# Performance work log

Hardware: AMD Instinct MI355X
Metric: run time of the kernel (lower is better)

Reference implementation:

```python
import jax, jax.numpy as jnp
import numpy as np

K, D = 512, 256

def setup_inputs() -> dict:
    key = jax.random.key(0)
    k1, k2 = jax.random.split(key)
    z_e = jax.random.normal(k1, (64, D, 32, 32), dtype=jnp.float32)
    # matches nn.Embedding weight init uniform_(-1/K, 1/K)
    codebook = jax.random.uniform(k2, (K, D), dtype=jnp.float32, minval=-1.0 / K, maxval=1.0 / K)
    return {"z_e": z_e, "codebook": codebook}

def reference(z_e, codebook):
    N, Dd, H, W = z_e.shape
    # NCHW -> (N*H*W, D) tokens
    x = jnp.transpose(z_e, (0, 2, 3, 1)).reshape(-1, Dd)
    x_sq = jnp.sum(x * x, axis=1, keepdims=True)            # [T, 1]
    w_sq = jnp.sum(codebook * codebook, axis=1)             # [K]
    dists = x_sq - 2.0 * (x @ codebook.T) + w_sq[None, :]   # [T, K]
    q = jnp.argmin(dists, axis=1)                           # [T]
    z_q = codebook[q]                                       # [T, D] gather
    z_q = z_q.reshape(N, H, W, Dd).transpose(0, 3, 1, 2)    # back to NCHW
    q = q.reshape(N, H, W).astype(jnp.int64)
    return (q, z_q)
```

## Files before the change

kernel.cpp:

```cpp
#include <hip/hip_runtime.h>
#include <float.h>
#include <math.h>


#define KCODES 512
#define DDIM   256
#define HWSZ   1024
#define TTOK   65536
#define TPB    128
#define NBLK   (TTOK / TPB)
#define NCHUNK 16
#define MARGIN 3.0e-4f
#define KINIT  0x00800000u

#define HW_OFF 65536
#define BK_OFF 67584
#define LDS_SZ 68096
#define WLC_OFF 49152
#define WLT_OFF 49168
#define WLK_OFF 49680
#define ZQ_PITCH 528

typedef short bf16x8 __attribute__((ext_vector_type(8)));
typedef float f32x16 __attribute__((ext_vector_type(16)));
typedef float f32x4  __attribute__((ext_vector_type(4)));

__device__ inline unsigned short bf16rne(float x) {
    union { float f; unsigned u; } a; a.f = x;
    unsigned r = a.u + (0x7fffu + ((a.u >> 16) & 1u));
    return (unsigned short)(r >> 16);
}
__device__ inline float bf16tof(unsigned short h) {
    union { unsigned u; float f; } b; b.u = ((unsigned)h) << 16; return b.f;
}

__device__ inline unsigned enc_key(float f, int code) {
    unsigned s = __float_as_uint(f);
    unsigned u = (s & 0x80000000u) ? ~s : (s | 0x80000000u);
    return (u & 0xFFFFFE00u) | (unsigned)code;
}
__device__ inline float dec_key(unsigned k) {
    unsigned u = k & 0xFFFFFE00u;
    unsigned s = (u & 0x80000000u) ? (u & 0x7FFFFFFFu) : ~u;
    return __uint_as_float(s);
}

__device__ __forceinline__ void top4k(unsigned k, unsigned kb[4]) {
    #pragma unroll
    for (int l = 0; l < 4; ++l) {
        const unsigned mx = k > kb[l] ? k : kb[l];
        const unsigned mn = k > kb[l] ? kb[l] : k;
        kb[l] = mx; k = mn;
    }
}
__device__ __forceinline__ void top8k(unsigned k, unsigned kb[8]) {
    #pragma unroll
    for (int l = 0; l < 8; ++l) {
        const unsigned mx = k > kb[l] ? k : kb[l];
        const unsigned mn = k > kb[l] ? kb[l] : k;
        kb[l] = mx; k = mn;
    }
}

__global__ __launch_bounds__(256) void vq_prep(const float* __restrict__ cb,
                                               unsigned char* __restrict__ wsw,
                                               float* __restrict__ wsq) {
    const int tid = threadIdx.x;
    const int gid = blockIdx.x * 256 + tid;
    {
        const int k = gid >> 5, o = gid & 31;
        const int d0 = o * 8, c = o >> 1, half = o & 1;
        unsigned hi[4], lo[4];
        #pragma unroll
        for (int jj = 0; jj < 4; ++jj) {
            float v0 = cb[k * DDIM + d0 + 2 * jj];
            float v1 = cb[k * DDIM + d0 + 2 * jj + 1];
            unsigned short h0 = bf16rne(v0), h1 = bf16rne(v1);
            unsigned short l0 = bf16rne(v0 - bf16tof(h0));
            unsigned short l1 = bf16rne(v1 - bf16tof(h1));
            hi[jj] = (unsigned)h0 | ((unsigned)h1 << 16);
            lo[jj] = (unsigned)l0 | ((unsigned)l1 << 16);
        }
        const int tile = k >> 5, lane2 = (k & 31) + 32 * half;
        *(uint4*)(wsw + ((size_t)((c * 2 + 0) * 16 + tile) * 1024) + lane2 * 16) = make_uint4(hi[0], hi[1], hi[2], hi[3]);
        *(uint4*)(wsw + ((size_t)((c * 2 + 1) * 16 + tile) * 1024) + lane2 * 16) = make_uint4(lo[0], lo[1], lo[2], lo[3]);
    }
    if (blockIdx.x < 32) {
        const int k = blockIdx.x * 16 + (tid >> 4);
        const int s = tid & 15, h2 = s >> 3, j2 = s & 7;
        const float* p = cb + (size_t)k * DDIM + h2 * 128 + j2;
        float v[16];
        #pragma unroll
        for (int i = 0; i < 16; ++i) v[i] = p[i * 8];
        float rr;
        {
#pragma clang fp contract(off)
            rr = v[0] * v[0];
            #pragma unroll
            for (int i = 1; i < 16; ++i) { float sq = v[i] * v[i]; rr = rr + sq; }
        }
        float t = rr;
        t = t + __shfl_xor(t, 1);
        t = t + __shfl_xor(t, 2);
        t = t + __shfl_xor(t, 4);
        t = t + __shfl_xor(t, 8);
        if (s == 0) wsq[k] = t;
    }
}

__global__ __launch_bounds__(512, 4) void vq_main(const float* __restrict__ z_e,
                                                  const float* __restrict__ cb,
                                                  const float* __restrict__ wsq,
                                                  const unsigned char* __restrict__ wsw,
                                                  float* __restrict__ out) {
    __shared__ __align__(16) unsigned char lds[LDS_SZ];

    const int tid = threadIdx.x;
    const int wv = tid >> 6, lane = tid & 63;
    const int tbase = blockIdx.x * TPB;
    const int n = tbase >> 10, hw0 = tbase & (HWSZ - 1);
    const float* zb = z_e + (size_t)n * (DDIM * HWSZ) + hw0;

    {
        const int tok = tid & 127, g = tid >> 7;
        const int mtS = tok >> 5;
        const int lbase = (tok & 31) * 16;
        #pragma unroll
        for (int o = 0; o < 8; ++o) {
            const int d0 = g * 64 + o * 8;
            float v[8];
            #pragma unroll
            for (int j = 0; j < 8; ++j) v[j] = zb[(size_t)(d0 + j) * HWSZ + tok];
            unsigned hi[4];
            #pragma unroll
            for (int jj = 0; jj < 4; ++jj) {
                unsigned short h0 = bf16rne(v[2 * jj]), h1 = bf16rne(v[2 * jj + 1]);
                hi[jj] = (unsigned)h0 | ((unsigned)h1 << 16);
            }
            const int c = d0 >> 4;
            const int off2 = lbase + 512 * ((d0 >> 3) & 1);
            *(uint4*)(lds + (mtS * 16 + c) * 1024 + off2) = make_uint4(hi[0], hi[1], hi[2], hi[3]);
        }
    }
    ((float*)(lds + HW_OFF))[tid] = 0.5f * wsq[tid];

    __syncthreads();

    const int hh = lane >> 5;
    const int ct0 = wv * 2;
    const float* hwsqL = (const float*)(lds + HW_OFF);
    unsigned* candp = (unsigned*)lds;

    #define LDW(c, p, t)   (*(const bf16x8*)(wsw + ((size_t)(((c) * 2 + (p)) * 16 + (t)) * 1024) + lane * 16))
    #define LDA(mm, c)     (*(const bf16x8*)(lds + ((mm) * 16 + (c)) * 1024 + lane * 16))

    unsigned kA[4], kB[4];
    #pragma unroll
    for (int pass = 0; pass < 2; ++pass) {
        const int mtA = 2 * pass, mtB = 2 * pass + 1;
        #pragma unroll
        for (int c = 0; c < 4; ++c) { kA[c] = KINIT; kB[c] = KINIT; }
        {
            f32x16 a00, a01, a10, a11;
            #pragma unroll
            for (int r = 0; r < 16; ++r) { a00[r] = 0.f; a01[r] = 0.f; a10[r] = 0.f; a11[r] = 0.f; }
            bf16x8 Xc[2][2], Wc[2][4];
            Xc[0][0] = LDA(mtA, 0); Xc[0][1] = LDA(mtB, 0);
            Wc[0][0] = LDW(0, 0, ct0);     Wc[0][1] = LDW(0, 1, ct0);
            Wc[0][2] = LDW(0, 0, ct0 + 1); Wc[0][3] = LDW(0, 1, ct0 + 1);
            #pragma unroll
            for (int c = 0; c < NCHUNK; ++c) {
                const int cur = c & 1, nxt = cur ^ 1;
                if (c + 1 < NCHUNK) {
                    Wc[nxt][0] = LDW(c + 1, 0, ct0);     Wc[nxt][1] = LDW(c + 1, 1, ct0);
                    Wc[nxt][2] = LDW(c + 1, 0, ct0 + 1); Wc[nxt][3] = LDW(c + 1, 1, ct0 + 1);
                    Xc[nxt][0] = LDA(mtA, c + 1); Xc[nxt][1] = LDA(mtB, c + 1);
                }
                a00 = __builtin_amdgcn_mfma_f32_32x32x16_bf16(Wc[cur][0], Xc[cur][0], a00, 0, 0, 0);
                a10 = __builtin_amdgcn_mfma_f32_32x32x16_bf16(Wc[cur][0], Xc[cur][1], a10, 0, 0, 0);
                a01 = __builtin_amdgcn_mfma_f32_32x32x16_bf16(Wc[cur][2], Xc[cur][0], a01, 0, 0, 0);
                a11 = __builtin_amdgcn_mfma_f32_32x32x16_bf16(Wc[cur][2], Xc[cur][1], a11, 0, 0, 0);
                a00 = __builtin_amdgcn_mfma_f32_32x32x16_bf16(Wc[cur][1], Xc[cur][0], a00, 0, 0, 0);
                a10 = __builtin_amdgcn_mfma_f32_32x32x16_bf16(Wc[cur][1], Xc[cur][1], a10, 0, 0, 0);
                a01 = __builtin_amdgcn_mfma_f32_32x32x16_bf16(Wc[cur][3], Xc[cur][0], a01, 0, 0, 0);
                a11 = __builtin_amdgcn_mfma_f32_32x32x16_bf16(Wc[cur][3], Xc[cur][1], a11, 0, 0, 0);
            }
            #pragma unroll
            for (int rq = 0; rq < 4; ++rq) {
                const f32x4 h40 = *(const f32x4*)(hwsqL + ct0 * 32 + rq * 8 + 4 * hh);
                const f32x4 h41 = *(const f32x4*)(hwsqL + (ct0 + 1) * 32 + rq * 8 + 4 * hh);
                #pragma unroll
                for (int rr = 0; rr < 4; ++rr) {
                    const int code0 = ct0 * 32 + rr + 8 * rq + 4 * hh;
                    const int code1 = (ct0 + 1) * 32 + rr + 8 * rq + 4 * hh;
                    top4k(enc_key(a00[rq * 4 + rr] - h40[rr], code0), kA);
                    top4k(enc_key(a01[rq * 4 + rr] - h41[rr], code1), kA);
                    top4k(enc_key(a10[rq * 4 + rr] - h40[rr], code0), kB);
                    top4k(enc_key(a11[rq * 4 + rr] - h41[rr], code1), kB);
                }
            }
        }
        {
            unsigned sb[4];
            #pragma unroll
            for (int c = 0; c < 4; ++c) sb[c] = __shfl_xor((int)kA[c], 32);
            #pragma unroll
            for (int c = 0; c < 4; ++c) top4k(sb[c], kA);
            #pragma unroll
            for (int c = 0; c < 4; ++c) sb[c] = __shfl_xor((int)kB[c], 32);
            #pragma unroll
            for (int c = 0; c < 4; ++c) top4k(sb[c], kB);
        }
        if (pass == 0) __syncthreads();
        if (lane < 32) {
            const int tokA = mtA * 32 + lane, tokB = mtB * 32 + lane;
            *(uint4*)(candp + (wv * 128 + tokA) * 4) = make_uint4(kA[0], kA[1], kA[2], kA[3]);
            *(uint4*)(candp + (wv * 128 + tokB) * 4) = make_uint4(kB[0], kB[1], kB[2], kB[3]);
        }
    }
    __syncthreads();

    int*      wlCnt = (int*)(lds + WLC_OFF);
    int*      wlTok = (int*)(lds + WLT_OFF);
    unsigned* wlK   = (unsigned*)(lds + WLK_OFF);
    int*      bkArr = (int*)(lds + BK_OFF);
    if (tid == 0) *wlCnt = 0;
    __syncthreads();

    if (tid < TPB) {
        unsigned kk[8];
        #pragma unroll
        for (int c = 0; c < 8; ++c) kk[c] = KINIT;
        #pragma unroll
        for (int w8 = 0; w8 < 8; ++w8) {
            const uint4 q4 = *(const uint4*)(candp + (w8 * 128 + tid) * 4);
            top8k(q4.x, kk); top8k(q4.y, kk); top8k(q4.z, kk); top8k(q4.w, kk);
        }
        const float g0 = dec_key(kk[0]), g1 = dec_key(kk[1]);
        if (g0 - g1 > MARGIN) {
            out[tbase + tid] = (float)(kk[0] & 511u);
            bkArr[tid] = (int)(kk[0] & 511u);
        } else {
            const int slot = atomicAdd(wlCnt, 1);
            wlTok[slot] = tid;
            #pragma unroll
            for (int c = 0; c < 8; ++c) wlK[slot * 8 + c] = kk[c];
        }
    }
    __syncthreads();

    {
        const int nIt = *wlCnt;
        for (int it = wv; it < nIt; it += 8) {
            const int tok = wlTok[it];
            const float g0 = dec_key(wlK[it * 8]);
            const float* xa = zb + tok;

            float xsq;
            {
                const int h2 = (lane >> 3) & 1, j2 = lane & 7;
                float v[16];
                if (lane < 16) {
                    #pragma unroll
                    for (int i = 0; i < 16; ++i)
                        v[i] = xa[(size_t)(h2 * 128 + i * 8 + j2) * HWSZ];
                } else {
                    #pragma unroll
                    for (int i = 0; i < 16; ++i) v[i] = 0.f;
                }
                float rr;
                {
#pragma clang fp contract(off)
                    rr = v[0] * v[0];
                    #pragma unroll
                    for (int i = 1; i < 16; ++i) { float sq = v[i] * v[i]; rr = rr + sq; }
                }
                float t = rr;
                t = t + __shfl_xor(t, 1);
                t = t + __shfl_xor(t, 2);
                t = t + __shfl_xor(t, 4);
                t = t + __shfl_xor(t, 8);
                xsq = __shfl(t, 0);
            }

            double xv[4];
            #pragma unroll
            for (int i = 0; i < 4; ++i)
                xv[i] = (double)xa[(size_t)(lane + 64 * i) * HWSZ];

            float bestd = FLT_MAX; int bestk = KCODES;
            for (int c = 0; c < 8; ++c) {
                const unsigned kc = wlK[it * 8 + c];
                const float gc = dec_key(kc);
                if (c > 0 && g0 - gc > MARGIN) break;
                const int idx = (int)(kc & 511u);
                const float* wr = cb + (size_t)idx * DDIM;
                double A = 0.0;
                #pragma unroll
                for (int i = 0; i < 4; ++i)
                    A = fma((double)wr[lane + 64 * i], xv[i], A);
                A = A + __shfl_xor(A, 1);
                A = A + __shfl_xor(A, 2);
                A = A + __shfl_xor(A, 4);
                A = A + __shfl_xor(A, 8);
                A = A + __shfl_xor(A, 16);
                A = A + __shfl_xor(A, 32);
                float dist;
                {
#pragma clang fp contract(off)
                    const float xw = (float)A;
                    const float t1 = xsq - 2.0f * xw;
                    dist = t1 + wsq[idx];
                }
                if (dist < bestd || (dist == bestd && idx < bestk)) { bestd = dist; bestk = idx; }
            }
            if (lane == 0) {
                out[tbase + tok] = (float)bestk;
                bkArr[tok] = bestk;
            }
        }
    }

    #pragma unroll
    for (int r = 0; r < 4; ++r) {
        const int rg = (r & 1) * 64;
        const int dh = (r >> 1) * 128;
        __syncthreads();
        {
            #pragma unroll
            for (int rr = 0; rr < 8; ++rr) {
                const int row = wv * 8 + rr;
                const int bk = bkArr[rg + row];
                const float2 vv = *(const float2*)(cb + (size_t)bk * DDIM + dh + lane * 2);
                *(float2*)(lds + row * ZQ_PITCH + lane * 8) = vv;
            }
        }
        __syncthreads();
        {
            const int tk = tid & 63, s = tid >> 6;
            float* zq = out + TTOK + (size_t)n * (DDIM * HWSZ) + hw0 + rg + tk;
            #pragma unroll
            for (int i = 0; i < 16; i += 4) {
                const f32x4 v = *(const f32x4*)(lds + tk * ZQ_PITCH + (s * 16 + i) * 4);
                #pragma unroll
                for (int j = 0; j < 4; ++j)
                    zq[(size_t)(dh + s * 16 + i + j) * HWSZ] = v[j];
            }
        }
    }
}

extern "C" void kernel_launch(void* const* d_in, const int* in_sizes, int n_in,
                              void* d_out, int out_size, void* d_ws, size_t ws_size,
                              hipStream_t stream) {
    const float* z_e = (const float*)d_in[0];
    const float* cb  = (const float*)d_in[1];
    float* out = (float*)d_out;
    float* wsq = (float*)d_ws;
    unsigned char* wsw = (unsigned char*)d_ws + 2048;

    vq_prep<<<64, 256, 0, stream>>>(cb, wsw, wsq);
    vq_main<<<NBLK, 512, 0, stream>>>(z_e, cb, wsq, wsw, out);
}
```

Before: 205.6 us.

## Halve tokens per block to cut LDS footprint and drop two-pass loop

Measured after the change: 193.0 us. 6.1% less time.

```diff
diff --git a/kernel.cpp b/kernel.cpp
--- a/kernel.cpp
+++ b/kernel.cpp
@@ -7,18 +7,15 @@
 #define DDIM   256
 #define HWSZ   1024
 #define TTOK   65536
-#define TPB    128
+#define TPB    64
 #define NBLK   (TTOK / TPB)
 #define NCHUNK 16
 #define MARGIN 3.0e-4f
 #define KINIT  0x00800000u
 
-#define HW_OFF 65536
-#define BK_OFF 67584
-#define LDS_SZ 68096
-#define WLC_OFF 49152
-#define WLT_OFF 49168
-#define WLK_OFF 49680
+#define HW_OFF 33792
+#define BK_OFF 35840
+#define LDS_SZ 36096
 #define ZQ_PITCH 528
 
 typedef short bf16x8 __attribute__((ext_vector_type(8)));
@@ -122,12 +119,12 @@
     const float* zb = z_e + (size_t)n * (DDIM * HWSZ) + hw0;
 
     {
-        const int tok = tid & 127, g = tid >> 7;
+        const int tok = tid & 63, g = tid >> 6;
         const int mtS = tok >> 5;
         const int lbase = (tok & 31) * 16;
         #pragma unroll
-        for (int o = 0; o < 8; ++o) {
-            const int d0 = g * 64 + o * 8;
+        for (int o = 0; o < 4; ++o) {
+            const int d0 = g * 32 + o * 8;
             float v[8];
             #pragma unroll
             for (int j = 0; j < 8; ++j) v[j] = zb[(size_t)(d0 + j) * HWSZ + tok];
@@ -149,81 +146,76 @@
     const int hh = lane >> 5;
     const int ct0 = wv * 2;
     const float* hwsqL = (const float*)(lds + HW_OFF);
-    unsigned* candp = (unsigned*)lds;
 
     #define LDW(c, p, t)   (*(const bf16x8*)(wsw + ((size_t)(((c) * 2 + (p)) * 16 + (t)) * 1024) + lane * 16))
     #define LDA(mm, c)     (*(const bf16x8*)(lds + ((mm) * 16 + (c)) * 1024 + lane * 16))
 
-    unsigned kA[4], kB[4];
-    #pragma unroll
-    for (int pass = 0; pass < 2; ++pass) {
-        const int mtA = 2 * pass, mtB = 2 * pass + 1;
-        #pragma unroll
-        for (int c = 0; c < 4; ++c) { kA[c] = KINIT; kB[c] = KINIT; }
-        {
-            f32x16 a00, a01, a10, a11;
-            #pragma unroll
-            for (int r = 0; r < 16; ++r) { a00[r] = 0.f; a01[r] = 0.f; a10[r] = 0.f; a11[r] = 0.f; }
-            bf16x8 Xc[2][2], Wc[2][4];
-            Xc[0][0] = LDA(mtA, 0); Xc[0][1] = LDA(mtB, 0);
-            Wc[0][0] = LDW(0, 0, ct0);     Wc[0][1] = LDW(0, 1, ct0);
-            Wc[0][2] = LDW(0, 0, ct0 + 1); Wc[0][3] = LDW(0, 1, ct0 + 1);
-            #pragma unroll
-            for (int c = 0; c < NCHUNK; ++c) {
-                const int cur = c & 1, nxt = cur ^ 1;
-                if (c + 1 < NCHUNK) {
-                    Wc[nxt][0] = LDW(c + 1, 0, ct0);     Wc[nxt][1] = LDW(c + 1, 1, ct0);
-                    Wc[nxt][2] = LDW(c + 1, 0, ct0 + 1); Wc[nxt][3] = LDW(c + 1, 1, ct0 + 1);
-                    Xc[nxt][0] = LDA(mtA, c + 1); Xc[nxt][1] = LDA(mtB, c + 1);
-                }
-                a00 = __builtin_amdgcn_mfma_f32_32x32x16_bf16(Wc[cur][0], Xc[cur][0], a00, 0, 0, 0);
-                a10 = __builtin_amdgcn_mfma_f32_32x32x16_bf16(Wc[cur][0], Xc[cur][1], a10, 0, 0, 0);
-                a01 = __builtin_amdgcn_mfma_f32_32x32x16_bf16(Wc[cur][2], Xc[cur][0], a01, 0, 0, 0);
-                a11 = __builtin_amdgcn_mfma_f32_32x32x16_bf16(Wc[cur][2], Xc[cur][1], a11, 0, 0, 0);
-                a00 = __builtin_amdgcn_mfma_f32_32x32x16_bf16(Wc[cur][1], Xc[cur][0], a00, 0, 0, 0);
-                a10 = __builtin_amdgcn_mfma_f32_32x32x16_bf16(Wc[cur][1], Xc[cur][1], a10, 0, 0, 0);
-                a01 = __builtin_amdgcn_mfma_f32_32x32x16_bf16(Wc[cur][3], Xc[cur][0], a01, 0, 0, 0);
-                a11 = __builtin_amdgcn_mfma_f32_32x32x16_bf16(Wc[cur][3], Xc[cur][1], a11, 0, 0, 0);
-            }
-            #pragma unroll
-            for (int rq = 0; rq < 4; ++rq) {
-                const f32x4 h40 = *(const f32x4*)(hwsqL + ct0 * 32 + rq * 8 + 4 * hh);
-                const f32x4 h41 = *(const f32x4*)(hwsqL + (ct0 + 1) * 32 + rq * 8 + 4 * hh);
-                #pragma unroll
-                for (int rr = 0; rr < 4; ++rr) {
-                    const int code0 = ct0 * 32 + rr + 8 * rq + 4 * hh;
-                    const int code1 = (ct0 + 1) * 32 + rr + 8 * rq + 4 * hh;
-                    top4k(enc_key(a00[rq * 4 + rr] - h40[rr], code0), kA);
-                    top4k(enc_key(a01[rq * 4 + rr] - h41[rr], code1), kA);
-                    top4k(enc_key(a10[rq * 4 + rr] - h40[rr], code0), kB);
-                    top4k(enc_key(a11[rq * 4 + rr] - h41[rr], code1), kB);
-                }
-            }
-        }
-        {
-            unsigned sb[4];
-            #pragma unroll
-            for (int c = 0; c < 4; ++c) sb[c] = __shfl_xor((int)kA[c], 32);
-            #pragma unroll
-            for (int c = 0; c < 4; ++c) top4k(sb[c], kA);
-            #pragma unroll
-            for (int c = 0; c < 4; ++c) sb[c] = __shfl_xor((int)kB[c], 32);
-            #pragma unroll
-            for (int c = 0; c < 4; ++c) top4k(sb[c], kB);
-        }
-        if (pass == 0) __syncthreads();
-        if (lane < 32) {
-            const int tokA = mtA * 32 + lane, tokB = mtB * 32 + lane;
-            *(uint4*)(candp + (wv * 128 + tokA) * 4) = make_uint4(kA[0], kA[1], kA[2], kA[3]);
-            *(uint4*)(candp + (wv * 128 + tokB) * 4) = make_uint4(kB[0], kB[1], kB[2], kB[3]);
-        }
-    }
+    unsigned kA[4] = {KINIT, KINIT, KINIT, KINIT};
+    unsigned kB[4] = {KINIT, KINIT, KINIT, KINIT};
+
+    {
+        f32x16 a00, a01, a10, a11;
+        #pragma unroll
+        for (int r = 0; r < 16; ++r) { a00[r] = 0.f; a01[r] = 0.f; a10[r] = 0.f; a11[r] = 0.f; }
+        bf16x8 Xc[2][2], Wc[2][4];
+        Xc[0][0] = LDA(0, 0); Xc[0][1] = LDA(1, 0);
+        Wc[0][0] = LDW(0, 0, ct0);     Wc[0][1] = LDW(0, 1, ct0);
+        Wc[0][2] = LDW(0, 0, ct0 + 1); Wc[0][3] = LDW(0, 1, ct0 + 1);
+        #pragma unroll
+        for (int c = 0; c < NCHUNK; ++c) {
+            const int cur = c & 1, nxt = cur ^ 1;
+            if (c + 1 < NCHUNK) {
+                Wc[nxt][0] = LDW(c + 1, 0, ct0);     Wc[nxt][1] = LDW(c + 1, 1, ct0);
+                Wc[nxt][2] = LDW(c + 1, 0, ct0 + 1); Wc[nxt][3] = LDW(c + 1, 1, ct0 + 1);
+                Xc[nxt][0] = LDA(0, c + 1); Xc[nxt][1] = LDA(1, c + 1);
+            }
+            a00 = __builtin_amdgcn_mfma_f32_32x32x16_bf16(Wc[cur][0], Xc[cur][0], a00, 0, 0, 0);
+            a10 = __builtin_amdgcn_mfma_f32_32x32x16_bf16(Wc[cur][0], Xc[cur][1], a10, 0, 0, 0);
+            a01 = __builtin_amdgcn_mfma_f32_32x32x16_bf16(Wc[cur][2], Xc[cur][0], a01, 0, 0, 0);
+            a11 = __builtin_amdgcn_mfma_f32_32x32x16_bf16(Wc[cur][2], Xc[cur][1], a11, 0, 0, 0);
+            a00 = __builtin_amdgcn_mfma_f32_32x32x16_bf16(Wc[cur][1], Xc[cur][0], a00, 0, 0, 0);
+            a10 = __builtin_amdgcn_mfma_f32_32x32x16_bf16(Wc[cur][1], Xc[cur][1], a10, 0, 0, 0);
+            a01 = __builtin_amdgcn_mfma_f32_32x32x16_bf16(Wc[cur][3], Xc[cur][0], a01, 0, 0, 0);
+            a11 = __builtin_amdgcn_mfma_f32_32x32x16_bf16(Wc[cur][3], Xc[cur][1], a11, 0, 0, 0);
+        }
+        #pragma unroll
+        for (int rq = 0; rq < 4; ++rq) {
+            const f32x4 h40 = *(const f32x4*)(hwsqL + ct0 * 32 + rq * 8 + 4 * hh);
+            const f32x4 h41 = *(const f32x4*)(hwsqL + (ct0 + 1) * 32 + rq * 8 + 4 * hh);
+            #pragma unroll
+            for (int rr = 0; rr < 4; ++rr) {
+                const int code0 = ct0 * 32 + rr + 8 * rq + 4 * hh;
+                const int code1 = (ct0 + 1) * 32 + rr + 8 * rq + 4 * hh;
+                top4k(enc_key(a00[rq * 4 + rr] - h40[rr], code0), kA);
+                top4k(enc_key(a01[rq * 4 + rr] - h41[rr], code1), kA);
+                top4k(enc_key(a10[rq * 4 + rr] - h40[rr], code0), kB);
+                top4k(enc_key(a11[rq * 4 + rr] - h41[rr], code1), kB);
+            }
+        }
+    }
+
+    {
+        unsigned sb[4];
+        #pragma unroll
+        for (int c = 0; c < 4; ++c) sb[c] = (unsigned)__shfl_xor((int)kA[c], 32);
+        #pragma unroll
+        for (int c = 0; c < 4; ++c) top4k(sb[c], kA);
+        #pragma unroll
+        for (int c = 0; c < 4; ++c) sb[c] = (unsigned)__shfl_xor((int)kB[c], 32);
+        #pragma unroll
+        for (int c = 0; c < 4; ++c) top4k(sb[c], kB);
+    }
+
     __syncthreads();
-
-    int*      wlCnt = (int*)(lds + WLC_OFF);
-    int*      wlTok = (int*)(lds + WLT_OFF);
-    unsigned* wlK   = (unsigned*)(lds + WLK_OFF);
+    unsigned* candp = (unsigned*)lds;
+    int*      wlCnt = (int*)(lds + 8192);
+    int*      wlTok = (int*)(lds + 8208);
+    unsigned* wlK   = (unsigned*)(lds + 8464);
     int*      bkArr = (int*)(lds + BK_OFF);
+    if (lane < 32) {
+        *(uint4*)(candp + (wv * 64 + lane) * 4)      = make_uint4(kA[0], kA[1], kA[2], kA[3]);
+        *(uint4*)(candp + (wv * 64 + 32 + lane) * 4) = make_uint4(kB[0], kB[1], kB[2], kB[3]);
+    }
     if (tid == 0) *wlCnt = 0;
     __syncthreads();
 
@@ -233,7 +225,7 @@
         for (int c = 0; c < 8; ++c) kk[c] = KINIT;
         #pragma unroll
         for (int w8 = 0; w8 < 8; ++w8) {
-            const uint4 q4 = *(const uint4*)(candp + (w8 * 128 + tid) * 4);
+            const uint4 q4 = *(const uint4*)(candp + (w8 * 64 + tid) * 4);
             top8k(q4.x, kk); top8k(q4.y, kk); top8k(q4.z, kk); top8k(q4.w, kk);
         }
         const float g0 = dec_key(kk[0]), g1 = dec_key(kk[1]);
@@ -322,29 +314,27 @@
     }
 
     #pragma unroll
-    for (int r = 0; r < 4; ++r) {
-        const int rg = (r & 1) * 64;
-        const int dh = (r >> 1) * 128;
+    for (int r = 0; r < 2; ++r) {
         __syncthreads();
         {
             #pragma unroll
             for (int rr = 0; rr < 8; ++rr) {
                 const int row = wv * 8 + rr;
-                const int bk = bkArr[rg + row];
-                const float2 vv = *(const float2*)(cb + (size_t)bk * DDIM + dh + lane * 2);
+                const int bk = bkArr[row];
+                const float2 vv = *(const float2*)(cb + (size_t)bk * DDIM + r * 128 + lane * 2);
                 *(float2*)(lds + row * ZQ_PITCH + lane * 8) = vv;
             }
         }
         __syncthreads();
         {
             const int tk = tid & 63, s = tid >> 6;
-            float* zq = out + TTOK + (size_t)n * (DDIM * HWSZ) + hw0 + rg + tk;
+            float* zq = out + TTOK + (size_t)n * (DDIM * HWSZ) + hw0 + tk;
             #pragma unroll
             for (int i = 0; i < 16; i += 4) {
                 const f32x4 v = *(const f32x4*)(lds + tk * ZQ_PITCH + (s * 16 + i) * 4);
                 #pragma unroll
                 for (int j = 0; j < 4; ++j)
-                    zq[(size_t)(dh + s * 16 + i + j) * HWSZ] = v[j];
+                    zq[(size_t)(r * 128 + s * 16 + i + j) * HWSZ] = v[j];
             }
         }
     }
```
